# Kernel tuning notes

Hardware: AMD Instinct MI355X
Metric: run time of the kernel (lower is better)

Reference implementation:

```python
import jax, jax.numpy as jnp
import numpy as np

EMBED_DIM = 512
KERNEL = 17


def setup_inputs() -> dict:
    key = jax.random.key(0)
    ks = jax.random.split(key, 5)
    B, L, C = 2, 8192, EMBED_DIM
    s = C ** -0.5
    x = jax.random.normal(ks[0], (B, L, C), dtype=jnp.float32)
    # weights stored as (in, out); equivalent to torch Linear weight.T
    w_qkv = jax.random.normal(ks[1], (C, 3 * C), dtype=jnp.float32) * s
    w_width = jax.random.normal(ks[2], (C, 1), dtype=jnp.float32) * s
    b_width = jax.random.normal(ks[3], (1,), dtype=jnp.float32) * 0.01
    w_out = jax.random.normal(ks[4], (C, C), dtype=jnp.float32) * s
    return {"x": x, "w_qkv": w_qkv, "w_width": w_width, "b_width": b_width, "w_out": w_out}


def reference(x, w_qkv, w_width, b_width, w_out):
    B, L, C = x.shape
    K = KERNEL
    half_k = K // 2
    scale = C ** -0.5

    qkv = x @ w_qkv                      # [B,L,3C]
    q, k, v = jnp.split(qkv, 3, axis=-1)

    # learned soft window width in [1, K]
    width = jax.nn.sigmoid(x @ w_width + b_width) * (K - 1) + 1.0   # [B,L,1]

    # sliding windows of k/v: pad along L then gather K-sized windows
    k_pad = jnp.pad(k, ((0, 0), (half_k, half_k), (0, 0)))
    v_pad = jnp.pad(v, ((0, 0), (half_k, half_k), (0, 0)))
    idx = jnp.arange(L)[:, None] + jnp.arange(K)[None, :]           # [L,K]
    k_win = k_pad[:, idx]                # [B,L,K,C]
    v_win = v_pad[:, idx]                # [B,L,K,C]

    scores = jnp.einsum('blc,blkc->blk', q, k_win) * scale          # [B,L,K]

    rel_pos = jnp.abs(jnp.arange(K, dtype=jnp.float32) - half_k)    # [K]
    soft_mask = jax.nn.sigmoid((width - rel_pos) * 5.0)             # [B,L,K]
    scores = scores - (1.0 - soft_mask) * 10000.0

    attn = jax.nn.softmax(scores, axis=-1)
    out = jnp.einsum('blk,blkc->blc', attn, v_win)                  # [B,L,C]
    return (out + v) @ w_out
```

## Files before the change

### kernel.cpp

```cpp
#include <hip/hip_runtime.h>

typedef unsigned short u16;
typedef unsigned int   u32;
typedef __attribute__((ext_vector_type(8))) short          shortx8;
typedef __attribute__((ext_vector_type(8))) unsigned short ushortx8;
typedef __attribute__((ext_vector_type(4))) float          floatx4;

#define AS1 __attribute__((address_space(1)))
#define AS3 __attribute__((address_space(3)))

#define SEG 8208
#define LV  16416

__device__ __forceinline__ float b2f(u16 v) {
  return __uint_as_float(((u32)v) << 16);
}
__device__ __forceinline__ u16 f2b(float f) {
  u32 u = __float_as_uint(f);
  u += 0x7FFF + ((u >> 16) & 1);
  return (u16)(u >> 16);
}
__device__ __forceinline__ void cp16(const void* g, void* l) {
  __builtin_amdgcn_global_load_lds((AS1 u32*)g, (AS3 u32*)l, 16, 0, 0);
}

__global__ __launch_bounds__(256)
void prep(const float* __restrict__ x, const float* __restrict__ w_width,
          const float* __restrict__ b_width, const float* __restrict__ w_qkv,
          const float* __restrict__ w_out, u16* __restrict__ xb,
          float* __restrict__ width, u16* __restrict__ wqkvT,
          u16* __restrict__ woutT, u16* __restrict__ Vt) {
  __shared__ u16 tile[32][33];
  const int b = blockIdx.x;
  if (b < 4096) {
    const int lane = threadIdx.x & 63;
    const int row  = b * 4 + (threadIdx.x >> 6);
    const float* xp = x + (size_t)row * 512 + lane * 8;
    floatx4 v0 = *(const floatx4*)xp;
    floatx4 v1 = *(const floatx4*)(xp + 4);
    floatx4 w0 = *(const floatx4*)(w_width + lane * 8);
    floatx4 w1 = *(const floatx4*)(w_width + lane * 8 + 4);
    float s = 0.f;
    ushortx8 o;
#pragma unroll
    for (int j = 0; j < 4; ++j) {
      s += v0[j] * w0[j] + v1[j] * w1[j];
      o[j] = f2b(v0[j]); o[4 + j] = f2b(v1[j]);
    }
    *(ushortx8*)(xb + (size_t)row * 512 + lane * 8) = o;
#pragma unroll
    for (int m = 32; m >= 1; m >>= 1) s += __shfl_xor(s, m, 64);
    if (lane == 0)
      width[row] = 16.f / (1.f + __expf(-(s + b_width[0]))) + 1.f;
  } else if (b < 5120) {
    const float* in; u16* out; int R, C, t;
    if (b < 4864) { in = w_qkv; out = wqkvT; R = 512; C = 1536; t = b - 4096; }
    else          { in = w_out; out = woutT; R = 512; C = 512;  t = b - 4864; }
    const int nbx = C / 32;
    const int cb = (t % nbx) * 32;
    const int rb = (t / nbx) * 32;
    const int tx = threadIdx.x & 31;
    const int ty = threadIdx.x >> 5;
#pragma unroll
    for (int i = 0; i < 32; i += 8)
      tile[ty + i][tx] = f2b(in[(size_t)(rb + ty + i) * C + cb + tx]);
    __syncthreads();
#pragma unroll
    for (int i = 0; i < 32; i += 8)
      out[(size_t)(cb + ty + i) * R + rb + tx] = tile[tx][ty + i];
  } else {
    const int idx = (b - 5120) * 256 + threadIdx.x;
    const int ch = idx >> 5;
    const int k  = idx & 31;
    const int seg = k >> 4;
    const int j   = k & 15;
    const int col = seg * SEG + (j < 8 ? j : 8192 + j);
    Vt[(size_t)ch * LV + col] = 0;
  }
}

template <int MODE>
__global__ __launch_bounds__(256, 3)
void gemm_bt(const u16* __restrict__ A, const u16* __restrict__ Bt,
             void* __restrict__ C0, u16* __restrict__ Kb, u16* __restrict__ Vt) {
  const int K = 512;
  __shared__ alignas(16) u16 lds[17408];
  u16* As = lds;
  u16* Bs = lds + 8192;
  const int tid  = threadIdx.x;
  const int lane = tid & 63;
  const int wave = tid >> 6;
  const int quad = lane >> 4;
  const int lr   = lane & 15;
  const int row0 = blockIdx.x * 128;
  const int col0 = blockIdx.y * 128;
  const int wr   = (wave >> 1) * 64;
  const int wc   = (wave & 1) * 64;

  floatx4 acc[4][4];
#pragma unroll
  for (int i = 0; i < 4; ++i)
#pragma unroll
    for (int j = 0; j < 4; ++j) acc[i][j] = (floatx4)0.0f;

  int srow[4], scol[4];
#pragma unroll
  for (int p = 0; p < 4; ++p) {
    int c = p * 256 + tid;
    srow[p] = c >> 3;
    scol[p] = ((c & 7) ^ (srow[p] & 7)) * 8;
  }
  const int swz = lr & 7;

  for (int k0 = 0; k0 < K; k0 += 64) {
#pragma unroll
    for (int p = 0; p < 4; ++p)
      cp16(A + (size_t)(row0 + srow[p]) * K + k0 + scol[p], &As[(p * 256 + tid) * 8]);
#pragma unroll
    for (int p = 0; p < 4; ++p)
      cp16(Bt + (size_t)(col0 + srow[p]) * K + k0 + scol[p], &Bs[(p * 256 + tid) * 8]);
    __syncthreads();

#pragma unroll
    for (int ks = 0; ks < 2; ++ks) {
      shortx8 af[4], bf[4];
#pragma unroll
      for (int mi = 0; mi < 4; ++mi)
        af[mi] = *(const shortx8*)
            &As[((wr + mi * 16 + lr) * 8 + ((ks * 4 + quad) ^ swz)) * 8];
#pragma unroll
      for (int ni = 0; ni < 4; ++ni)
        bf[ni] = *(const shortx8*)
            &Bs[((wc + ni * 16 + lr) * 8 + ((ks * 4 + quad) ^ swz)) * 8];
#pragma unroll
      for (int mi = 0; mi < 4; ++mi)
#pragma unroll
        for (int ni = 0; ni < 4; ++ni)
          acc[mi][ni] = __builtin_amdgcn_mfma_f32_16x16x32_bf16(
              af[mi], bf[ni], acc[mi][ni], 0, 0, 0);
    }
    __syncthreads();
  }

  if constexpr (MODE == 1) {
    if (col0 < 1024) {
      u16* dst = (col0 < 512) ? (u16*)C0 : Kb;
      const int cb = col0 & 511;
#pragma unroll
      for (int mi = 0; mi < 4; ++mi)
#pragma unroll
        for (int ni = 0; ni < 4; ++ni)
#pragma unroll
          for (int r = 0; r < 4; ++r)
            lds[(wr + mi * 16 + quad * 4 + r) * 136 + wc + ni * 16 + lr] =
                f2b(acc[mi][ni][r]);
      __syncthreads();
      const int rr = tid >> 4, cc = (tid & 15) * 8;
#pragma unroll
      for (int it = 0; it < 8; ++it) {
        int row = it * 16 + rr;
        *(ushortx8*)(dst + (size_t)(row0 + row) * 512 + cb + cc) =
            *(const ushortx8*)&lds[row * 136 + cc];
      }
    } else {
      const int cb = col0 - 1024;
      const int bb = row0 >> 13, pib0 = row0 & 8191;
#pragma unroll
      for (int mi = 0; mi < 4; ++mi)
#pragma unroll
        for (int ni = 0; ni < 4; ++ni)
#pragma unroll
          for (int r = 0; r < 4; ++r)
            lds[(wc + ni * 16 + lr) * 136 + wr + mi * 16 + quad * 4 + r] =
                f2b(acc[mi][ni][r]);
      __syncthreads();
      const int rr = tid >> 4, cc = (tid & 15) * 8;
#pragma unroll
      for (int it = 0; it < 8; ++it) {
        int chl = it * 16 + rr;
        ushortx8 v = *(const ushortx8*)&lds[chl * 136 + cc];
        *(ushortx8*)(Vt + (size_t)(cb + chl) * LV + (size_t)bb * SEG + 8 + pib0 + cc) = v;
      }
    }
  } else {
    float* Cf = (float*)C0;
#pragma unroll
    for (int mi = 0; mi < 4; ++mi)
#pragma unroll
      for (int ni = 0; ni < 4; ++ni)
#pragma unroll
        for (int r = 0; r < 4; ++r) {
          int row = row0 + wr + mi * 16 + quad * 4 + r;
          int col = col0 + wc + ni * 16 + lr;
          Cf[(size_t)row * 512 + col] = acc[mi][ni][r];
        }
  }
}

__global__ __launch_bounds__(256, 1)
void attn_fused(const u16* __restrict__ Q, const u16* __restrict__ Kb,
                const u16* __restrict__ Vt, const float* __restrict__ width,
                const u16* __restrict__ woutT, float* __restrict__ Out) {
  __shared__ alignas(16) u16 Osw[64 * 256];
  __shared__ alignas(16) u16 P[4][16][32];
  const int tid  = threadIdx.x;
  const int lane = tid & 63;
  const int wave = tid >> 6;
  const int quad = lane >> 4;
  const int lr   = lane & 15;
  const int p0   = blockIdx.x * 64;
  const int pw   = p0 + wave * 16;
  const int pibw = pw & 8191;
  const int bb   = pw >> 13;
  const size_t cb0 = (size_t)bb * SEG + pibw;

  shortx8 vfA[16];
#pragma unroll
  for (int ctl = 0; ctl < 16; ++ctl)
    vfA[ctl] = *(const shortx8*)(Vt + (size_t)(ctl * 16 + lr) * LV +
                                 cb0 + quad * 8);

  floatx4 s0 = (floatx4)0.0f, s1 = (floatx4)0.0f;
#pragma unroll 4
  for (int s = 0; s < 16; ++s) {
    const int k0 = s * 32 + quad * 8;
    shortx8 af = *(const shortx8*)(Q  + (size_t)(pw + lr) * 512 + k0);
    shortx8 f0 = *(const shortx8*)(Kb + (ptrdiff_t)(pw - 8 + lr) * 512 + k0);
    shortx8 f1 = *(const shortx8*)(Kb + (ptrdiff_t)(pw + 8 + lr) * 512 + k0);
    s0 = __builtin_amdgcn_mfma_f32_16x16x32_bf16(af, f0, s0, 0, 0, 0);
    s1 = __builtin_amdgcn_mfma_f32_16x16x32_bf16(af, f1, s1, 0, 0, 0);
  }

  {
    const float scale = 0.044194173824159216f;
    floatx4 wv = *(const floatx4*)(width + pw + quad * 4);
#pragma unroll
    for (int r = 0; r < 4; ++r) {
      const int row = quad * 4 + r;
      const int d0  = lr - row;
      const int d1  = d0 + 16;
      const int jb0 = pibw + lr - 8;
      const int jb1 = jb0 + 16;
      float rel0 = fabsf((float)(d0 - 8));
      float rel1 = fabsf((float)(d1 - 8));
      float mk0 = 1.f / (1.f + __expf(-5.f * (wv[r] - rel0)));
      float mk1 = 1.f / (1.f + __expf(-5.f * (wv[r] - rel1)));
      float val0 = (d0 >= 0)
          ? (((unsigned)jb0 < 8192u ? s0[r] * scale : 0.f) - (1.f - mk0) * 10000.f)
          : -1e30f;
      float val1 = (d1 <= 16)
          ? (((unsigned)jb1 < 8192u ? s1[r] * scale : 0.f) - (1.f - mk1) * 10000.f)
          : -1e30f;
      float mx = fmaxf(val0, val1);
#pragma unroll
      for (int m = 8; m >= 1; m >>= 1) mx = fmaxf(mx, __shfl_xor(mx, m, 64));
      float e0 = __expf(val0 - mx), e1 = __expf(val1 - mx);
      float sum = e0 + e1;
#pragma unroll
      for (int m = 8; m >= 1; m >>= 1) sum += __shfl_xor(sum, m, 64);
      const float inv = 1.f / sum;
      P[wave][row][lr]      = f2b(e0 * inv + (d0 == 8 ? 1.f : 0.f));
      P[wave][row][lr + 16] = f2b(e1 * inv + (d1 == 8 ? 1.f : 0.f));
    }
  }
  shortx8 pf = *(const shortx8*)&P[wave][lr][quad * 8];

  const int wc = wave * 128;
  floatx4 acc[4][8];
#pragma unroll
  for (int mi = 0; mi < 4; ++mi)
#pragma unroll
    for (int ni = 0; ni < 8; ++ni) acc[mi][ni] = (floatx4)0.0f;

  shortx8 vfB[16];
#pragma unroll
  for (int ctl = 0; ctl < 16; ++ctl)
    vfB[ctl] = *(const shortx8*)(Vt + (size_t)(256 + ctl * 16 + lr) * LV +
                                 cb0 + quad * 8);

#pragma unroll
  for (int ctl = 0; ctl < 16; ++ctl) {
    floatx4 o = __builtin_amdgcn_mfma_f32_16x16x32_bf16(pf, vfA[ctl],
                                                        (floatx4)0.0f, 0, 0, 0);
    const int c = ctl * 2 + (lr >> 3);
#pragma unroll
    for (int r = 0; r < 4; ++r) {
      const int row = wave * 16 + quad * 4 + r;
      Osw[row * 256 + (((c & ~7) | ((c & 7) ^ (row & 7))) << 3) + (lr & 7)] =
          f2b(o[r]);
    }
  }
  __syncthreads();

  {
    shortx8 bcur[8], bnxt[8];
#pragma unroll
    for (int ni = 0; ni < 8; ++ni)
      bcur[ni] = *(const shortx8*)(woutT + (size_t)(wc + ni * 16 + lr) * 512 +
                                   quad * 8);
    for (int ksl = 0; ksl < 8; ++ksl) {
      if (ksl < 7) {
#pragma unroll
        for (int ni = 0; ni < 8; ++ni)
          bnxt[ni] = *(const shortx8*)(woutT +
                       (size_t)(wc + ni * 16 + lr) * 512 +
                       (ksl + 1) * 32 + quad * 8);
      }
      shortx8 afr[4];
#pragma unroll
      for (int mi = 0; mi < 4; ++mi) {
        const int row = mi * 16 + lr;
        const int c = ksl * 4 + quad;
        afr[mi] = *(const shortx8*)
            &Osw[row * 256 + (((c & ~7) | ((c & 7) ^ (row & 7))) << 3)];
      }
#pragma unroll
      for (int mi = 0; mi < 4; ++mi)
#pragma unroll
        for (int ni = 0; ni < 8; ++ni)
          acc[mi][ni] = __builtin_amdgcn_mfma_f32_16x16x32_bf16(
              afr[mi], bcur[ni], acc[mi][ni], 0, 0, 0);
      if (ksl < 7) {
#pragma unroll
        for (int ni = 0; ni < 8; ++ni) bcur[ni] = bnxt[ni];
      }
    }
  }
  __syncthreads();

#pragma unroll
  for (int ctl = 0; ctl < 16; ++ctl) {
    floatx4 o = __builtin_amdgcn_mfma_f32_16x16x32_bf16(pf, vfB[ctl],
                                                        (floatx4)0.0f, 0, 0, 0);
    const int c = ctl * 2 + (lr >> 3);
#pragma unroll
    for (int r = 0; r < 4; ++r) {
      const int row = wave * 16 + quad * 4 + r;
      Osw[row * 256 + (((c & ~7) | ((c & 7) ^ (row & 7))) << 3) + (lr & 7)] =
          f2b(o[r]);
    }
  }
  __syncthreads();

  {
    shortx8 bcur[8], bnxt[8];
#pragma unroll
    for (int ni = 0; ni < 8; ++ni)
      bcur[ni] = *(const shortx8*)(woutT + (size_t)(wc + ni * 16 + lr) * 512 +
                                   256 + quad * 8);
    for (int ksl = 0; ksl < 8; ++ksl) {
      if (ksl < 7) {
#pragma unroll
        for (int ni = 0; ni < 8; ++ni)
          bnxt[ni] = *(const shortx8*)(woutT +
                       (size_t)(wc + ni * 16 + lr) * 512 +
                       256 + (ksl + 1) * 32 + quad * 8);
      }
      shortx8 afr[4];
#pragma unroll
      for (int mi = 0; mi < 4; ++mi) {
        const int row = mi * 16 + lr;
        const int c = ksl * 4 + quad;
        afr[mi] = *(const shortx8*)
            &Osw[row * 256 + (((c & ~7) | ((c & 7) ^ (row & 7))) << 3)];
      }
#pragma unroll
      for (int mi = 0; mi < 4; ++mi)
#pragma unroll
        for (int ni = 0; ni < 8; ++ni)
          acc[mi][ni] = __builtin_amdgcn_mfma_f32_16x16x32_bf16(
              afr[mi], bcur[ni], acc[mi][ni], 0, 0, 0);
      if (ksl < 7) {
#pragma unroll
        for (int ni = 0; ni < 8; ++ni) bcur[ni] = bnxt[ni];
      }
    }
  }

#pragma unroll
  for (int mi = 0; mi < 4; ++mi)
#pragma unroll
    for (int ni = 0; ni < 8; ++ni)
#pragma unroll
      for (int r = 0; r < 4; ++r)
        Out[(size_t)(p0 + mi * 16 + quad * 4 + r) * 512 + wc + ni * 16 + lr] =
            acc[mi][ni][r];
}

extern "C" void kernel_launch(void* const* d_in, const int* in_sizes, int n_in,
                              void* d_out, int out_size, void* d_ws, size_t ws_size,
                              hipStream_t stream) {
  const float* x       = (const float*)d_in[0];
  const float* w_qkv   = (const float*)d_in[1];
  const float* w_width = (const float*)d_in[2];
  const float* b_width = (const float*)d_in[3];
  const float* w_out   = (const float*)d_in[4];
  float* out = (float*)d_out;

  const int M = 16384, N3 = 1536;
  char* ws = (char*)d_ws;
  u16*   xb    = (u16*)(ws);
  u16*   Qb    = (u16*)(ws + 16777216);
  u16*   Kb    = (u16*)(ws + 33554432 + 8192);
  u16*   Vt    = (u16*)(ws + 50348032);
  u16*   wqkvT = (u16*)(ws + 67158016);
  u16*   woutT = (u16*)(ws + 68730880);
  float* width = (float*)(ws + 69255168);

  prep<<<dim3(5184), dim3(256), 0, stream>>>(x, w_width, b_width, w_qkv, w_out,
                                             xb, width, wqkvT, woutT, Vt);
  gemm_bt<1><<<dim3(M / 128, N3 / 128), dim3(256), 0, stream>>>(xb, wqkvT, Qb,
                                                                Kb, Vt);
  attn_fused<<<dim3(M / 64), dim3(256), 0, stream>>>(Qb, Kb, Vt, width, woutT,
                                                     out);
}
```

Measured before the change: 155.2 us.

## Fold Wq·Wk^T into a precomputed matrix and use x as attention keys

```diff
diff --git a/kernel.cpp b/kernel.cpp
--- a/kernel.cpp
+++ b/kernel.cpp
@@ -28,13 +28,101 @@
 void prep(const float* __restrict__ x, const float* __restrict__ w_width,
           const float* __restrict__ b_width, const float* __restrict__ w_qkv,
           const float* __restrict__ w_out, u16* __restrict__ xb,
-          float* __restrict__ width, u16* __restrict__ wqkvT,
+          float* __restrict__ width, u16* __restrict__ BtAll,
           u16* __restrict__ woutT, u16* __restrict__ Vt) {
+  __shared__ alignas(16) u16 shb[17408];
   __shared__ u16 tile[32][33];
   const int b = blockIdx.x;
-  if (b < 4096) {
+  if (b < 16) {
+    const int t    = b;
+    const int row0 = (t >> 2) * 128;
+    const int col0 = (t & 3) * 128;
+    const int tid  = threadIdx.x;
+    const int lane = tid & 63;
+    const int wave = tid >> 6;
+    const int quad = lane >> 4;
+    const int lr   = lane & 15;
+    const int wr   = (wave >> 1) * 64;
+    const int wc   = (wave & 1) * 64;
+    u16* As = shb;
+    u16* Bs = shb + 8192;
+
+    floatx4 acc[4][4];
+#pragma unroll
+    for (int i = 0; i < 4; ++i)
+#pragma unroll
+      for (int j = 0; j < 4; ++j) acc[i][j] = (floatx4)0.0f;
+
+    int srow[4], scol[4];
+#pragma unroll
+    for (int p = 0; p < 4; ++p) {
+      int c = p * 256 + tid;
+      srow[p] = c >> 3;
+      scol[p] = ((c & 7) ^ (srow[p] & 7)) * 8;
+    }
+    const int swz = lr & 7;
+
+    for (int k0 = 0; k0 < 512; k0 += 64) {
+#pragma unroll
+      for (int p = 0; p < 4; ++p) {
+        const float* ga = w_qkv + (size_t)(row0 + srow[p]) * 1536 + k0 + scol[p];
+        floatx4 a0 = *(const floatx4*)ga;
+        floatx4 a1 = *(const floatx4*)(ga + 4);
+        ushortx8 o;
+#pragma unroll
+        for (int j = 0; j < 4; ++j) { o[j] = f2b(a0[j]); o[4 + j] = f2b(a1[j]); }
+        *(ushortx8*)&As[(p * 256 + tid) * 8] = o;
+      }
+#pragma unroll
+      for (int p = 0; p < 4; ++p) {
+        const float* gb = w_qkv + (size_t)(col0 + srow[p]) * 1536 + 512 + k0 + scol[p];
+        floatx4 b0 = *(const floatx4*)gb;
+        floatx4 b1 = *(const floatx4*)(gb + 4);
+        ushortx8 o;
+#pragma unroll
+        for (int j = 0; j < 4; ++j) { o[j] = f2b(b0[j]); o[4 + j] = f2b(b1[j]); }
+        *(ushortx8*)&Bs[(p * 256 + tid) * 8] = o;
+      }
+      __syncthreads();
+#pragma unroll
+      for (int ks = 0; ks < 2; ++ks) {
+        shortx8 af[4], bf[4];
+#pragma unroll
+        for (int mi = 0; mi < 4; ++mi)
+          af[mi] = *(const shortx8*)
+              &As[((wr + mi * 16 + lr) * 8 + ((ks * 4 + quad) ^ swz)) * 8];
+#pragma unroll
+        for (int ni = 0; ni < 4; ++ni)
+          bf[ni] = *(const shortx8*)
+              &Bs[((wc + ni * 16 + lr) * 8 + ((ks * 4 + quad) ^ swz)) * 8];
+#pragma unroll
+        for (int mi = 0; mi < 4; ++mi)
+#pragma unroll
+          for (int ni = 0; ni < 4; ++ni)
+            acc[mi][ni] = __builtin_amdgcn_mfma_f32_16x16x32_bf16(
+                af[mi], bf[ni], acc[mi][ni], 0, 0, 0);
+      }
+      __syncthreads();
+    }
+#pragma unroll
+    for (int mi = 0; mi < 4; ++mi)
+#pragma unroll
+      for (int ni = 0; ni < 4; ++ni)
+#pragma unroll
+        for (int r = 0; r < 4; ++r)
+          shb[(wc + ni * 16 + lr) * 136 + wr + mi * 16 + quad * 4 + r] =
+              f2b(acc[mi][ni][r]);
+    __syncthreads();
+    const int rr = tid >> 4, cc = (tid & 15) * 8;
+#pragma unroll
+    for (int it = 0; it < 8; ++it) {
+      int chl = it * 16 + rr;
+      *(ushortx8*)(BtAll + (size_t)(col0 + chl) * 512 + row0 + cc) =
+          *(const ushortx8*)&shb[chl * 136 + cc];
+    }
+  } else if (b < 4112) {
     const int lane = threadIdx.x & 63;
-    const int row  = b * 4 + (threadIdx.x >> 6);
+    const int row  = (b - 16) * 4 + (threadIdx.x >> 6);
     const float* xp = x + (size_t)row * 512 + lane * 8;
     floatx4 v0 = *(const floatx4*)xp;
     floatx4 v1 = *(const floatx4*)(xp + 4);
@@ -52,13 +140,14 @@
     for (int m = 32; m >= 1; m >>= 1) s += __shfl_xor(s, m, 64);
     if (lane == 0)
       width[row] = 16.f / (1.f + __expf(-(s + b_width[0]))) + 1.f;
-  } else if (b < 5120) {
-    const float* in; u16* out; int R, C, t;
-    if (b < 4864) { in = w_qkv; out = wqkvT; R = 512; C = 1536; t = b - 4096; }
-    else          { in = w_out; out = woutT; R = 512; C = 512;  t = b - 4864; }
-    const int nbx = C / 32;
-    const int cb = (t % nbx) * 32;
-    const int rb = (t / nbx) * 32;
+  } else if (b < 4624) {
+    const float* in = (b < 4368) ? w_qkv : w_out;
+    const int C  = (b < 4368) ? 1536 : 512;
+    const int t  = (b < 4368) ? (b - 4112) : (b - 4368);
+    const int cbo = (b < 4368) ? 1024 : 0;
+    u16* out = (b < 4368) ? (BtAll + 512 * 512) : woutT;
+    const int cb = cbo + (t & 15) * 32;
+    const int rb = (t >> 4) * 32;
     const int tx = threadIdx.x & 31;
     const int ty = threadIdx.x >> 5;
 #pragma unroll
@@ -67,9 +156,9 @@
     __syncthreads();
 #pragma unroll
     for (int i = 0; i < 32; i += 8)
-      out[(size_t)(cb + ty + i) * R + rb + tx] = tile[tx][ty + i];
+      out[(size_t)(cb - cbo + ty + i) * 512 + rb + tx] = tile[tx][ty + i];
   } else {
-    const int idx = (b - 5120) * 256 + threadIdx.x;
+    const int idx = (b - 4624) * 256 + threadIdx.x;
     const int ch = idx >> 5;
     const int k  = idx & 31;
     const int seg = k >> 4;
@@ -79,10 +168,9 @@
   }
 }
 
-template <int MODE>
 __global__ __launch_bounds__(256, 3)
-void gemm_bt(const u16* __restrict__ A, const u16* __restrict__ Bt,
-             void* __restrict__ C0, u16* __restrict__ Kb, u16* __restrict__ Vt) {
+void gemm_qv(const u16* __restrict__ A, const u16* __restrict__ Bt,
+             u16* __restrict__ Qb, u16* __restrict__ Vt) {
   const int K = 512;
   __shared__ alignas(16) u16 lds[17408];
   u16* As = lds;
@@ -142,63 +230,48 @@
     __syncthreads();
   }
 
-  if constexpr (MODE == 1) {
-    if (col0 < 1024) {
-      u16* dst = (col0 < 512) ? (u16*)C0 : Kb;
-      const int cb = col0 & 511;
-#pragma unroll
-      for (int mi = 0; mi < 4; ++mi)
-#pragma unroll
-        for (int ni = 0; ni < 4; ++ni)
-#pragma unroll
-          for (int r = 0; r < 4; ++r)
-            lds[(wr + mi * 16 + quad * 4 + r) * 136 + wc + ni * 16 + lr] =
-                f2b(acc[mi][ni][r]);
-      __syncthreads();
-      const int rr = tid >> 4, cc = (tid & 15) * 8;
-#pragma unroll
-      for (int it = 0; it < 8; ++it) {
-        int row = it * 16 + rr;
-        *(ushortx8*)(dst + (size_t)(row0 + row) * 512 + cb + cc) =
-            *(const ushortx8*)&lds[row * 136 + cc];
-      }
-    } else {
-      const int cb = col0 - 1024;
-      const int bb = row0 >> 13, pib0 = row0 & 8191;
-#pragma unroll
-      for (int mi = 0; mi < 4; ++mi)
-#pragma unroll
-        for (int ni = 0; ni < 4; ++ni)
-#pragma unroll
-          for (int r = 0; r < 4; ++r)
-            lds[(wc + ni * 16 + lr) * 136 + wr + mi * 16 + quad * 4 + r] =
-                f2b(acc[mi][ni][r]);
-      __syncthreads();
-      const int rr = tid >> 4, cc = (tid & 15) * 8;
-#pragma unroll
-      for (int it = 0; it < 8; ++it) {
-        int chl = it * 16 + rr;
-        ushortx8 v = *(const ushortx8*)&lds[chl * 136 + cc];
-        *(ushortx8*)(Vt + (size_t)(cb + chl) * LV + (size_t)bb * SEG + 8 + pib0 + cc) = v;
-      }
+  if (col0 < 512) {
+    const int cb = col0;
+#pragma unroll
+    for (int mi = 0; mi < 4; ++mi)
+#pragma unroll
+      for (int ni = 0; ni < 4; ++ni)
+#pragma unroll
+        for (int r = 0; r < 4; ++r)
+          lds[(wr + mi * 16 + quad * 4 + r) * 136 + wc + ni * 16 + lr] =
+              f2b(acc[mi][ni][r]);
+    __syncthreads();
+    const int rr = tid >> 4, cc = (tid & 15) * 8;
+#pragma unroll
+    for (int it = 0; it < 8; ++it) {
+      int row = it * 16 + rr;
+      *(ushortx8*)(Qb + (size_t)(row0 + row) * 512 + cb + cc) =
+          *(const ushortx8*)&lds[row * 136 + cc];
     }
   } else {
-    float* Cf = (float*)C0;
+    const int cb = col0 - 512;
+    const int bb = row0 >> 13, pib0 = row0 & 8191;
 #pragma unroll
     for (int mi = 0; mi < 4; ++mi)
 #pragma unroll
       for (int ni = 0; ni < 4; ++ni)
 #pragma unroll
-        for (int r = 0; r < 4; ++r) {
-          int row = row0 + wr + mi * 16 + quad * 4 + r;
-          int col = col0 + wc + ni * 16 + lr;
-          Cf[(size_t)row * 512 + col] = acc[mi][ni][r];
-        }
+        for (int r = 0; r < 4; ++r)
+          lds[(wc + ni * 16 + lr) * 136 + wr + mi * 16 + quad * 4 + r] =
+              f2b(acc[mi][ni][r]);
+    __syncthreads();
+    const int rr = tid >> 4, cc = (tid & 15) * 8;
+#pragma unroll
+    for (int it = 0; it < 8; ++it) {
+      int chl = it * 16 + rr;
+      ushortx8 v = *(const ushortx8*)&lds[chl * 136 + cc];
+      *(ushortx8*)(Vt + (size_t)(cb + chl) * LV + (size_t)bb * SEG + 8 + pib0 + cc) = v;
+    }
   }
 }
 
 __global__ __launch_bounds__(256, 1)
-void attn_fused(const u16* __restrict__ Q, const u16* __restrict__ Kb,
+void attn_fused(const u16* __restrict__ Q, const u16* __restrict__ Kx,
                 const u16* __restrict__ Vt, const float* __restrict__ width,
                 const u16* __restrict__ woutT, float* __restrict__ Out) {
   __shared__ alignas(16) u16 Osw[64 * 256];
@@ -225,8 +298,8 @@
   for (int s = 0; s < 16; ++s) {
     const int k0 = s * 32 + quad * 8;
     shortx8 af = *(const shortx8*)(Q  + (size_t)(pw + lr) * 512 + k0);
-    shortx8 f0 = *(const shortx8*)(Kb + (ptrdiff_t)(pw - 8 + lr) * 512 + k0);
-    shortx8 f1 = *(const shortx8*)(Kb + (ptrdiff_t)(pw + 8 + lr) * 512 + k0);
+    shortx8 f0 = *(const shortx8*)(Kx + (ptrdiff_t)(pw - 8 + lr) * 512 + k0);
+    shortx8 f1 = *(const shortx8*)(Kx + (ptrdiff_t)(pw + 8 + lr) * 512 + k0);
     s0 = __builtin_amdgcn_mfma_f32_16x16x32_bf16(af, f0, s0, 0, 0, 0);
     s1 = __builtin_amdgcn_mfma_f32_16x16x32_bf16(af, f1, s1, 0, 0, 0);
   }
@@ -397,20 +470,18 @@
   const float* w_out   = (const float*)d_in[4];
   float* out = (float*)d_out;
 
-  const int M = 16384, N3 = 1536;
+  const int M = 16384;
   char* ws = (char*)d_ws;
-  u16*   xb    = (u16*)(ws);
-  u16*   Qb    = (u16*)(ws + 16777216);
-  u16*   Kb    = (u16*)(ws + 33554432 + 8192);
-  u16*   Vt    = (u16*)(ws + 50348032);
-  u16*   wqkvT = (u16*)(ws + 67158016);
-  u16*   woutT = (u16*)(ws + 68730880);
-  float* width = (float*)(ws + 69255168);
-
-  prep<<<dim3(5184), dim3(256), 0, stream>>>(x, w_width, b_width, w_qkv, w_out,
-                                             xb, width, wqkvT, woutT, Vt);
-  gemm_bt<1><<<dim3(M / 128, N3 / 128), dim3(256), 0, stream>>>(xb, wqkvT, Qb,
-                                                                Kb, Vt);
-  attn_fused<<<dim3(M / 64), dim3(256), 0, stream>>>(Qb, Kb, Vt, width, woutT,
+  u16*   xb    = (u16*)(ws + 8192);
+  u16*   Qb    = (u16*)(ws + 16785408);
+  u16*   Vt    = (u16*)(ws + 33562624);
+  u16*   BtAll = (u16*)(ws + 50372608);
+  u16*   woutT = (u16*)(ws + 51421184);
+  float* width = (float*)(ws + 51945472);
+
+  prep<<<dim3(4688), dim3(256), 0, stream>>>(x, w_width, b_width, w_qkv, w_out,
+                                             xb, width, BtAll, woutT, Vt);
+  gemm_qv<<<dim3(M / 128, 8), dim3(256), 0, stream>>>(xb, BtAll, Qb, Vt);
+  attn_fused<<<dim3(M / 64), dim3(256), 0, stream>>>(Qb, xb, Vt, width, woutT,
                                                      out);
 }
```

Result: no change. 155.4 us (+0.1%).
